# Performance work log

Measured on AMD Instinct MI355X. Metric: run time of the kernel, lower is better.

## Reference

```python
import jax, jax.numpy as jnp
import numpy as np

N_NODES = 100000
N_EDGES = 3200000
NFEAT = 512
HIDDEN = 256
NCLASS = 64
K = 10
ALPHA = 0.1


def setup_inputs() -> dict:
    key = jax.random.key(0)
    ks = jax.random.split(key, 5)
    x = jax.random.normal(ks[0], (N_NODES, NFEAT), dtype=jnp.float32)
    edge_index = jax.random.randint(ks[1], (2, N_EDGES), 0, N_NODES, dtype=jnp.int64)
    W1 = jax.random.normal(ks[2], (NFEAT, HIDDEN), dtype=jnp.float32) * (1.0 / np.sqrt(NFEAT))
    b1 = jnp.zeros((HIDDEN,), dtype=jnp.float32)
    W2 = jax.random.normal(ks[3], (HIDDEN, NCLASS), dtype=jnp.float32) * (1.0 / np.sqrt(HIDDEN))
    b2 = jnp.zeros((NCLASS,), dtype=jnp.float32)
    # PPR initialization of GPR coefficients: alpha*(1-alpha)^k, last = (1-alpha)^K
    temp_np = ALPHA * (1.0 - ALPHA) ** np.arange(K + 1)
    temp_np[-1] = (1.0 - ALPHA) ** K
    temp = jnp.asarray(temp_np, dtype=jnp.float32)
    return {"x": x, "edge_index": edge_index, "W1": W1, "b1": b1, "W2": W2, "b2": b2, "temp": temp}


def reference(x, edge_index, W1, b1, W2, b2, temp):
    N = x.shape[0]
    # --- gcn_norm: add self-loops, symmetric normalization ---
    loop = jnp.arange(N, dtype=edge_index.dtype)
    row = jnp.concatenate([edge_index[0], loop])  # source nodes
    col = jnp.concatenate([edge_index[1], loop])  # target nodes
    ones = jnp.ones(row.shape[0], dtype=x.dtype)
    deg = jax.ops.segment_sum(ones, col, num_segments=N)
    dinv = jnp.where(deg > 0, jax.lax.rsqrt(deg), jnp.zeros((), x.dtype))
    norm = dinv[row] * dinv[col]  # [E+N]

    # --- MLP (eval mode: dropout is identity) ---
    h = jax.nn.relu(x @ W1 + b1) @ W2 + b2  # [N, nclass]

    # --- GPR propagation: hidden = sum_k temp[k] * (Ahat^k h) ---
    hidden = h * temp[0]
    for k in range(K):
        h = jax.ops.segment_sum(norm[:, None] * h[row], col, num_segments=N)
        hidden = hidden + temp[k + 1] * h

    return jax.nn.log_softmax(hidden, axis=1)
```

## Files before the change

kernel.cpp:

```cpp
#include <hip/hip_runtime.h>
#include <hip/hip_bf16.h>
#include <math.h>

#define N_NODES 100000
#define N_EDGES 3200000
#define NFEAT   512
#define HIDDEN  256
#define NCLASS  64
#define K_HOPS  10
#define NPART   8
#define PART_SZ ((N_NODES + NPART - 1) / NPART)

typedef unsigned short bfbits;
typedef __attribute__((ext_vector_type(8))) short short8x;
typedef __attribute__((ext_vector_type(4))) float float4x;

__device__ __forceinline__ float bf2f(bfbits u) {
    union { unsigned int i; float f; } v; v.i = ((unsigned int)u) << 16; return v.f;
}
__device__ __forceinline__ bfbits f2bf(float f) {
    union { float f; unsigned int i; } v; v.f = f;
    unsigned int b = v.i + 0x7FFFu + ((v.i >> 16) & 1u);
    return (bfbits)(b >> 16);
}
__device__ __forceinline__ float2 unpack2(unsigned int u) {
    float2 r;
    union { unsigned int i; float f; } a, b;
    a.i = (u & 0xFFFFu) << 16; b.i = u & 0xFFFF0000u;
    r.x = a.f; r.y = b.f; return r;
}
__device__ __forceinline__ unsigned int pack2(float x, float y) {
    return ((unsigned int)f2bf(x)) | (((unsigned int)f2bf(y)) << 16);
}


__global__ void init_kernel(int* __restrict__ degi, int* __restrict__ cursor, int n) {
    int i = blockIdx.x * blockDim.x + threadIdx.x;
    if (i < n) { degi[i] = 1; cursor[i] = 0; }
}

__global__ void count_kernel(const int* __restrict__ col, int* __restrict__ degi, int e) {
    int i = blockIdx.x * blockDim.x + threadIdx.x;
    if (i < e) atomicAdd(&degi[col[i]], 1);
}

__global__ void dinv_kernel(const int* __restrict__ degi, float* __restrict__ dinv, int n) {
    int i = blockIdx.x * blockDim.x + threadIdx.x;
    if (i < n) dinv[i] = rsqrtf((float)degi[i]);
}

#define SCAN_NB 256
#define SCAN_NT 256

__global__ __launch_bounds__(SCAN_NT) void scan_phase1(const int* __restrict__ degi,
                                                       int* __restrict__ blocksums, int n) {
    int chunk = (n + SCAN_NB - 1) / SCAN_NB;
    int beg = blockIdx.x * chunk;
    int end = min(beg + chunk, n);
    int tid = threadIdx.x;
    int s = 0;
    for (int i = beg + tid; i < end; i += SCAN_NT) s += degi[i] - 1;
    __shared__ int wsum[SCAN_NT / 64];
#pragma unroll
    for (int o = 32; o > 0; o >>= 1) s += __shfl_xor(s, o, 64);
    if ((tid & 63) == 0) wsum[tid >> 6] = s;
    __syncthreads();
    if (tid == 0) {
        int t = 0;
#pragma unroll
        for (int w = 0; w < SCAN_NT / 64; ++w) t += wsum[w];
        blocksums[blockIdx.x] = t;
    }
}

__global__ __launch_bounds__(SCAN_NB) void scan_phase2(const int* __restrict__ blocksums,
                                                       int* __restrict__ blockbase) {
    __shared__ int t[SCAN_NB];
    int tid = threadIdx.x;
    t[tid] = blocksums[tid];
    __syncthreads();
    for (int d = 1; d < SCAN_NB; d <<= 1) {
        int v = (tid >= d) ? t[tid - d] : 0;
        __syncthreads();
        t[tid] += v;
        __syncthreads();
    }
    blockbase[tid] = (tid > 0) ? t[tid - 1] : 0;
}

__global__ __launch_bounds__(SCAN_NT) void scan_phase3(const int* __restrict__ degi,
                                                       const int* __restrict__ blockbase,
                                                       int* __restrict__ offs, int n) {
    __shared__ int tsum[SCAN_NT];
    int chunk = (n + SCAN_NB - 1) / SCAN_NB;
    int beg = blockIdx.x * chunk;
    int end = min(beg + chunk, n);
    int tid = threadIdx.x;
    int sub = (chunk + SCAN_NT - 1) / SCAN_NT;
    int tb = beg + tid * sub;
    int te = min(tb + sub, end);
    int s = 0;
    for (int i = tb; i < te; ++i) s += degi[i] - 1;
    tsum[tid] = s;
    __syncthreads();
    for (int d = 1; d < SCAN_NT; d <<= 1) {
        int v = (tid >= d) ? tsum[tid - d] : 0;
        __syncthreads();
        tsum[tid] += v;
        __syncthreads();
    }
    int run = blockbase[blockIdx.x] + ((tid > 0) ? tsum[tid - 1] : 0);
    for (int i = tb; i < te; ++i) { offs[i] = run; run += degi[i] - 1; }
    if (blockIdx.x == SCAN_NB - 1 && tid == SCAN_NT - 1)
        offs[n] = blockbase[blockIdx.x] + tsum[SCAN_NT - 1];
}

__global__ __launch_bounds__(256) void scatter_part(const int* __restrict__ row,
                                                    const int* __restrict__ col,
                                                    const int* __restrict__ offs,
                                                    int* __restrict__ cursor,
                                                    int* __restrict__ srcs, int e) {
    int part = blockIdx.x & (NPART - 1);
    int blk  = blockIdx.x >> 3;
    int nthr = (gridDim.x >> 3) * blockDim.x;
    int lo = part * PART_SZ, hi = lo + PART_SZ;
    for (int i = blk * blockDim.x + threadIdx.x; i < e; i += nthr) {
        int c = col[i];
        int r = row[i];
        if (c >= lo && c < hi) {
            int p = offs[c] + atomicAdd(&cursor[c], 1);
            srcs[p] = r;
        }
    }
}

__global__ __launch_bounds__(256) void transpose_cast(const float* __restrict__ src,
                                                      bfbits* __restrict__ dst,
                                                      int K, int N) {
    __shared__ float tile[32][33];
    int kt = blockIdx.x * 32, nt = blockIdx.y * 32;
    int c = threadIdx.x & 31, r0 = threadIdx.x >> 5;
#pragma unroll
    for (int i = 0; i < 4; ++i) {
        int r = r0 + i * 8;
        tile[r][c] = src[(size_t)(kt + r) * N + nt + c];
    }
    __syncthreads();
#pragma unroll
    for (int i = 0; i < 4; ++i) {
        int r = r0 + i * 8;
        dst[(size_t)(nt + r) * K + kt + c] = f2bf(tile[c][r]);
    }
}

#define LDP 40

__global__ __launch_bounds__(512) void gemm1_mfma(const float* __restrict__ X,
                                                  const bfbits* __restrict__ W1T,
                                                  const float* __restrict__ bias,
                                                  bfbits* __restrict__ H, int M) {
    __shared__ short x_lds[128 * LDP];
    __shared__ short w_lds[256 * LDP];
    int tid = threadIdx.x;
    int wave = tid >> 6, lane = tid & 63;
    int l15 = lane & 15, quad = lane >> 4;
    int fslot = wave & 3, nslot = wave >> 2;
    int m0 = blockIdx.x * 128;

    float4x acc[4][4];
#pragma unroll
    for (int i = 0; i < 4; ++i)
#pragma unroll
        for (int j = 0; j < 4; ++j) acc[i][j] = (float4x){0.f, 0.f, 0.f, 0.f};

    for (int kb = 0; kb < NFEAT; kb += 32) {
#pragma unroll
        for (int c = 0; c < 2; ++c) {
            int qid = tid + c * 512;
            int node = qid >> 3;
            int k0 = (qid & 7) * 4;
            int row = m0 + node;
            float4 v = make_float4(0.f, 0.f, 0.f, 0.f);
            if (row < M) v = *reinterpret_cast<const float4*>(X + (size_t)row * NFEAT + kb + k0);
            ushort4 u;
            u.x = f2bf(v.x); u.y = f2bf(v.y); u.z = f2bf(v.z); u.w = f2bf(v.w);
            *reinterpret_cast<ushort4*>(&x_lds[node * LDP + k0]) = u;
        }
#pragma unroll
        for (int c = 0; c < 2; ++c) {
            int qid = tid + c * 512;
            int feat = qid >> 2;
            int k0 = (qid & 3) * 8;
            uint4 w = *reinterpret_cast<const uint4*>(W1T + (size_t)feat * NFEAT + kb + k0);
            *reinterpret_cast<uint4*>(&w_lds[feat * LDP + k0]) = w;
        }
        __syncthreads();
        short8x af[4], bf[4];
#pragma unroll
        for (int t = 0; t < 4; ++t) {
            af[t] = *reinterpret_cast<const short8x*>(&w_lds[(fslot * 64 + t * 16 + l15) * LDP + quad * 8]);
            bf[t] = *reinterpret_cast<const short8x*>(&x_lds[(nslot * 64 + t * 16 + l15) * LDP + quad * 8]);
        }
#pragma unroll
        for (int ft = 0; ft < 4; ++ft)
#pragma unroll
            for (int nt = 0; nt < 4; ++nt)
                acc[ft][nt] = __builtin_amdgcn_mfma_f32_16x16x32_bf16(af[ft], bf[nt], acc[ft][nt], 0, 0, 0);
        __syncthreads();
    }
#pragma unroll
    for (int ft = 0; ft < 4; ++ft) {
        int f = fslot * 64 + ft * 16 + quad * 4;
        float4 b = *reinterpret_cast<const float4*>(bias + f);
#pragma unroll
        for (int nt = 0; nt < 4; ++nt) {
            int node = m0 + nslot * 64 + nt * 16 + l15;
            if (node >= M) continue;
            float4x a = acc[ft][nt];
            ushort4 u;
            u.x = f2bf(fmaxf(a.x + b.x, 0.f));
            u.y = f2bf(fmaxf(a.y + b.y, 0.f));
            u.z = f2bf(fmaxf(a.z + b.z, 0.f));
            u.w = f2bf(fmaxf(a.w + b.w, 0.f));
            *reinterpret_cast<ushort4*>(H + (size_t)node * HIDDEN + f) = u;
        }
    }
}

__global__ __launch_bounds__(256) void gemm2_mfma(const bfbits* __restrict__ Hm,
                                                  const bfbits* __restrict__ W2T,
                                                  const float* __restrict__ bias,
                                                  const float* __restrict__ dinv,
                                                  bfbits* __restrict__ g0,
                                                  float* __restrict__ S,
                                                  const float* __restrict__ temp, int M) {
    __shared__ short h_lds[256 * LDP];
    __shared__ short w_lds[64 * LDP];
    int tid = threadIdx.x;
    int wave = tid >> 6, lane = tid & 63;
    int l15 = lane & 15, quad = lane >> 4;
    int nslot = wave;
    int m0 = blockIdx.x * 256;

    float4x acc[4][4];
#pragma unroll
    for (int i = 0; i < 4; ++i)
#pragma unroll
        for (int j = 0; j < 4; ++j) acc[i][j] = (float4x){0.f, 0.f, 0.f, 0.f};

    for (int kb = 0; kb < HIDDEN; kb += 32) {
#pragma unroll
        for (int c = 0; c < 4; ++c) {
            int qid = tid + c * 256;
            int node = qid >> 2;
            int k0 = (qid & 3) * 8;
            int row = m0 + node;
            uint4 v = make_uint4(0u, 0u, 0u, 0u);
            if (row < M) v = *reinterpret_cast<const uint4*>(Hm + (size_t)row * HIDDEN + kb + k0);
            *reinterpret_cast<uint4*>(&h_lds[node * LDP + k0]) = v;
        }
        {
            int feat = tid >> 2;
            int k0 = (tid & 3) * 8;
            uint4 w = *reinterpret_cast<const uint4*>(W2T + (size_t)feat * HIDDEN + kb + k0);
            *reinterpret_cast<uint4*>(&w_lds[feat * LDP + k0]) = w;
        }
        __syncthreads();
        short8x af[4], bf[4];
#pragma unroll
        for (int t = 0; t < 4; ++t) {
            af[t] = *reinterpret_cast<const short8x*>(&w_lds[(t * 16 + l15) * LDP + quad * 8]);
            bf[t] = *reinterpret_cast<const short8x*>(&h_lds[(nslot * 64 + t * 16 + l15) * LDP + quad * 8]);
        }
#pragma unroll
        for (int ft = 0; ft < 4; ++ft)
#pragma unroll
            for (int nt = 0; nt < 4; ++nt)
                acc[ft][nt] = __builtin_amdgcn_mfma_f32_16x16x32_bf16(af[ft], bf[nt], acc[ft][nt], 0, 0, 0);
        __syncthreads();
    }
    float t0 = temp[0];
#pragma unroll
    for (int nt = 0; nt < 4; ++nt) {
        int node = m0 + nslot * 64 + nt * 16 + l15;
        if (node >= M) continue;
        float di = dinv[node];
        float s0 = t0 / di;
#pragma unroll
        for (int ft = 0; ft < 4; ++ft) {
            int f = ft * 16 + quad * 4;
            float4 b = *reinterpret_cast<const float4*>(bias + f);
            float4x a = acc[ft][nt];
            float4 v = make_float4(a.x + b.x, a.y + b.y, a.z + b.z, a.w + b.w);
            ushort4 u;
            u.x = f2bf(di * v.x); u.y = f2bf(di * v.y);
            u.z = f2bf(di * v.z); u.w = f2bf(di * v.w);
            *reinterpret_cast<ushort4*>(g0 + (size_t)node * NCLASS + f) = u;
            float4 sv = make_float4(s0 * v.x, s0 * v.y, s0 * v.z, s0 * v.w);
            *reinterpret_cast<float4*>(S + (size_t)node * 64 + f) = sv;
        }
    }
}

__global__ __launch_bounds__(256) void propagate_kernel(const int* __restrict__ offs,
                                                        const int* __restrict__ srcs,
                                                        const float* __restrict__ dinv,
                                                        const uint2* __restrict__ gin,
                                                        uint2* __restrict__ gout,
                                                        float* __restrict__ S,
                                                        const float* __restrict__ temp,
                                                        int kidx, int n) {
    int node = (blockIdx.x * blockDim.x + threadIdx.x) >> 6;
    int lane = threadIdx.x & 63;
    if (node >= n) return;
    int q = lane >> 4, sub = lane & 15;
    float tk = temp[kidx];
    int beg = offs[node], end = offs[node + 1];

    uint2 gs = gin[(size_t)node * 16 + sub];
    float4 acc = make_float4(0.f, 0.f, 0.f, 0.f);
    if (q == 0) {
        float2 lo = unpack2(gs.x), hi = unpack2(gs.y);
        acc = make_float4(lo.x, lo.y, hi.x, hi.y);
    }

    int e = beg;
    for (; e + 16 <= end; e += 16) {
#pragma unroll
        for (int j = 0; j < 4; ++j) {
            int s = srcs[e + j * 4 + q];
            uint2 u = gin[(size_t)s * 16 + sub];
            float2 lo = unpack2(u.x), hi = unpack2(u.y);
            acc.x += lo.x; acc.y += lo.y; acc.z += hi.x; acc.w += hi.y;
        }
    }
    for (; e < end; e += 4) {
        int idx = e + q;
        int sidx = (idx < end) ? idx : e;
        int s = srcs[sidx];
        uint2 u = gin[(size_t)s * 16 + sub];
        if (idx < end) {
            float2 lo = unpack2(u.x), hi = unpack2(u.y);
            acc.x += lo.x; acc.y += lo.y; acc.z += hi.x; acc.w += hi.y;
        }
    }

    acc.x += __shfl_xor(acc.x, 16, 64); acc.y += __shfl_xor(acc.y, 16, 64);
    acc.z += __shfl_xor(acc.z, 16, 64); acc.w += __shfl_xor(acc.w, 16, 64);
    acc.x += __shfl_xor(acc.x, 32, 64); acc.y += __shfl_xor(acc.y, 32, 64);
    acc.z += __shfl_xor(acc.z, 32, 64); acc.w += __shfl_xor(acc.w, 32, 64);

    if (q == 0) {
        float di = dinv[node];
        float dd = di * di;
        gout[(size_t)node * 16 + sub] =
            make_uint2(pack2(dd * acc.x, dd * acc.y), pack2(dd * acc.z, dd * acc.w));
        float4* Sp = reinterpret_cast<float4*>(S + (size_t)node * 64 + sub * 4);
        float4 sv = *Sp;
        sv.x += tk * acc.x; sv.y += tk * acc.y;
        sv.z += tk * acc.z; sv.w += tk * acc.w;
        *Sp = sv;
    }
}

__global__ __launch_bounds__(256) void logsoftmax_kernel(const float* __restrict__ S,
                                                         const float* __restrict__ dinv,
                                                         float* __restrict__ out, int n) {
    int node = (blockIdx.x * blockDim.x + threadIdx.x) >> 6;
    int lane = threadIdx.x & 63;
    if (node >= n) return;
    float v = dinv[node] * S[(size_t)node * 64 + lane];
    float m = v;
#pragma unroll
    for (int o = 32; o > 0; o >>= 1) m = fmaxf(m, __shfl_xor(m, o, 64));
    float ex = expf(v - m);
    float s = ex;
#pragma unroll
    for (int o = 32; o > 0; o >>= 1) s += __shfl_xor(s, o, 64);
    out[(size_t)node * 64 + lane] = v - m - logf(s);
}


extern "C" void kernel_launch(void* const* d_in, const int* in_sizes, int n_in,
                              void* d_out, int out_size, void* d_ws, size_t ws_size,
                              hipStream_t stream) {
    const float* x    = (const float*)d_in[0];
    const int*   ei   = (const int*)d_in[1];
    const int*   row  = ei;
    const int*   col  = ei + N_EDGES;
    const float* W1   = (const float*)d_in[2];
    const float* b1   = (const float*)d_in[3];
    const float* W2   = (const float*)d_in[4];
    const float* b2   = (const float*)d_in[5];
    const float* temp = (const float*)d_in[6];
    float*       out  = (float*)d_out;

    char* ws = (char*)d_ws;
    size_t off = 0;
    auto alloc = [&](size_t bytes) -> void* {
        void* p = ws + off;
        off += (bytes + 255) & ~(size_t)255;
        return p;
    };
    int*    degi   = (int*)   alloc((size_t)N_NODES * 4);
    float*  dinv   = (float*) alloc((size_t)N_NODES * 4);
    int*    offs   = (int*)   alloc((size_t)(N_NODES + 1) * 4);
    int*    cursor = (int*)   alloc((size_t)N_NODES * 4);
    int*    srcs   = (int*)   alloc((size_t)N_EDGES * 4);
    int*    bsums  = (int*)   alloc((size_t)SCAN_NB * 4);
    int*    bbase  = (int*)   alloc((size_t)SCAN_NB * 4);
    bfbits* W1T    = (bfbits*)alloc((size_t)HIDDEN * NFEAT * 2);
    bfbits* W2T    = (bfbits*)alloc((size_t)NCLASS * HIDDEN * 2);
    bfbits* h_mlp  = (bfbits*)alloc((size_t)N_NODES * HIDDEN * 2);
    bfbits* g_a    = (bfbits*)alloc((size_t)N_NODES * NCLASS * 2);
    bfbits* g_b    = (bfbits*)alloc((size_t)N_NODES * NCLASS * 2);
    float*  S      = (float*) alloc((size_t)N_NODES * NCLASS * 4);

    init_kernel<<<(N_NODES + 255) / 256, 256, 0, stream>>>(degi, cursor, N_NODES);
    count_kernel<<<(N_EDGES + 255) / 256, 256, 0, stream>>>(col, degi, N_EDGES);
    dinv_kernel<<<(N_NODES + 255) / 256, 256, 0, stream>>>(degi, dinv, N_NODES);
    scan_phase1<<<SCAN_NB, SCAN_NT, 0, stream>>>(degi, bsums, N_NODES);
    scan_phase2<<<1, SCAN_NB, 0, stream>>>(bsums, bbase);
    scan_phase3<<<SCAN_NB, SCAN_NT, 0, stream>>>(degi, bbase, offs, N_NODES);
    scatter_part<<<2048, 256, 0, stream>>>(row, col, offs, cursor, srcs, N_EDGES);

    dim3 gt1(NFEAT / 32, HIDDEN / 32);
    transpose_cast<<<gt1, 256, 0, stream>>>(W1, W1T, NFEAT, HIDDEN);
    dim3 gt2(HIDDEN / 32, NCLASS / 32);
    transpose_cast<<<gt2, 256, 0, stream>>>(W2, W2T, HIDDEN, NCLASS);

    gemm1_mfma<<<(N_NODES + 127) / 128, 512, 0, stream>>>(x, W1T, b1, h_mlp, N_NODES);
    gemm2_mfma<<<(N_NODES + 255) / 256, 256, 0, stream>>>(h_mlp, W2T, b2, dinv, g_a, S,
                                                          temp, N_NODES);

    int pgrid = (N_NODES * 64 + 255) / 256;
    for (int k = 0; k < K_HOPS; ++k) {
        bfbits* gi = (k & 1) ? g_b : g_a;
        bfbits* go = (k & 1) ? g_a : g_b;
        propagate_kernel<<<pgrid, 256, 0, stream>>>(offs, srcs, dinv,
                                                    (const uint2*)gi, (uint2*)go, S,
                                                    temp, k + 1, N_NODES);
    }

    logsoftmax_kernel<<<pgrid, 256, 0, stream>>>(S, dinv, out, N_NODES);
}
```

Before: 1.357 ms.

## Bucket CSR neighbor lists by source-node range to improve gather locality

Builds the CSR with four virtual buckets per destination node, keyed by which quarter of the source-node range each edge comes from. Within a node's neighbor list, sources are then grouped by region, so concurrent gathers in the propagation hops hit a smaller working set in cache. Edge index loads in the count and scatter kernels become nontemporal. In exchange the count, scan and cursor arrays grow fourfold and the count kernel also has to read the row indices.

```diff
diff --git a/kernel.cpp b/kernel.cpp
--- a/kernel.cpp
+++ b/kernel.cpp
@@ -10,6 +10,9 @@
 #define K_HOPS  10
 #define NPART   8
 #define PART_SZ ((N_NODES + NPART - 1) / NPART)
+#define NTILE   4
+#define TQ      25000
+#define NVIRT   (N_NODES * NTILE)
 
 typedef unsigned short bfbits;
 typedef __attribute__((ext_vector_type(8))) short short8x;
@@ -34,32 +37,41 @@
 }
 
 
-__global__ void init_kernel(int* __restrict__ degi, int* __restrict__ cursor, int n) {
+__global__ void init_kernel(int* __restrict__ bcnt, int* __restrict__ cursor, int n) {
     int i = blockIdx.x * blockDim.x + threadIdx.x;
-    if (i < n) { degi[i] = 1; cursor[i] = 0; }
-}
-
-__global__ void count_kernel(const int* __restrict__ col, int* __restrict__ degi, int e) {
+    if (i < n) { bcnt[i] = 0; cursor[i] = 0; }
+}
+
+__global__ void count_kernel(const int* __restrict__ row, const int* __restrict__ col,
+                             int* __restrict__ bcnt, int e) {
     int i = blockIdx.x * blockDim.x + threadIdx.x;
-    if (i < e) atomicAdd(&degi[col[i]], 1);
-}
-
-__global__ void dinv_kernel(const int* __restrict__ degi, float* __restrict__ dinv, int n) {
+    if (i < e) {
+        int r = __builtin_nontemporal_load(row + i);
+        int c = __builtin_nontemporal_load(col + i);
+        atomicAdd(&bcnt[c * NTILE + r / TQ], 1);
+    }
+}
+
+__global__ void dinv_kernel(const int* __restrict__ bcnt, float* __restrict__ dinv, int n) {
     int i = blockIdx.x * blockDim.x + threadIdx.x;
-    if (i < n) dinv[i] = rsqrtf((float)degi[i]);
+    if (i < n) {
+        int d = 1 + bcnt[i * NTILE] + bcnt[i * NTILE + 1] + bcnt[i * NTILE + 2]
+                  + bcnt[i * NTILE + 3];
+        dinv[i] = rsqrtf((float)d);
+    }
 }
 
 #define SCAN_NB 256
 #define SCAN_NT 256
 
-__global__ __launch_bounds__(SCAN_NT) void scan_phase1(const int* __restrict__ degi,
+__global__ __launch_bounds__(SCAN_NT) void scan_phase1(const int* __restrict__ bcnt,
                                                        int* __restrict__ blocksums, int n) {
     int chunk = (n + SCAN_NB - 1) / SCAN_NB;
     int beg = blockIdx.x * chunk;
     int end = min(beg + chunk, n);
     int tid = threadIdx.x;
     int s = 0;
-    for (int i = beg + tid; i < end; i += SCAN_NT) s += degi[i] - 1;
+    for (int i = beg + tid; i < end; i += SCAN_NT) s += bcnt[i];
     __shared__ int wsum[SCAN_NT / 64];
 #pragma unroll
     for (int o = 32; o > 0; o >>= 1) s += __shfl_xor(s, o, 64);
@@ -88,7 +100,7 @@
     blockbase[tid] = (tid > 0) ? t[tid - 1] : 0;
 }
 
-__global__ __launch_bounds__(SCAN_NT) void scan_phase3(const int* __restrict__ degi,
+__global__ __launch_bounds__(SCAN_NT) void scan_phase3(const int* __restrict__ bcnt,
                                                        const int* __restrict__ blockbase,
                                                        int* __restrict__ offs, int n) {
     __shared__ int tsum[SCAN_NT];
@@ -100,7 +112,7 @@
     int tb = beg + tid * sub;
     int te = min(tb + sub, end);
     int s = 0;
-    for (int i = tb; i < te; ++i) s += degi[i] - 1;
+    for (int i = tb; i < te; ++i) s += bcnt[i];
     tsum[tid] = s;
     __syncthreads();
     for (int d = 1; d < SCAN_NT; d <<= 1) {
@@ -110,14 +122,14 @@
         __syncthreads();
     }
     int run = blockbase[blockIdx.x] + ((tid > 0) ? tsum[tid - 1] : 0);
-    for (int i = tb; i < te; ++i) { offs[i] = run; run += degi[i] - 1; }
+    for (int i = tb; i < te; ++i) { offs[i] = run; run += bcnt[i]; }
     if (blockIdx.x == SCAN_NB - 1 && tid == SCAN_NT - 1)
         offs[n] = blockbase[blockIdx.x] + tsum[SCAN_NT - 1];
 }
 
 __global__ __launch_bounds__(256) void scatter_part(const int* __restrict__ row,
                                                     const int* __restrict__ col,
-                                                    const int* __restrict__ offs,
+                                                    const int* __restrict__ offs2,
                                                     int* __restrict__ cursor,
                                                     int* __restrict__ srcs, int e) {
     int part = blockIdx.x & (NPART - 1);
@@ -125,10 +137,11 @@
     int nthr = (gridDim.x >> 3) * blockDim.x;
     int lo = part * PART_SZ, hi = lo + PART_SZ;
     for (int i = blk * blockDim.x + threadIdx.x; i < e; i += nthr) {
-        int c = col[i];
-        int r = row[i];
+        int c = __builtin_nontemporal_load(col + i);
+        int r = __builtin_nontemporal_load(row + i);
         if (c >= lo && c < hi) {
-            int p = offs[c] + atomicAdd(&cursor[c], 1);
+            int vk = c * NTILE + r / TQ;
+            int p = offs2[vk] + atomicAdd(&cursor[vk], 1);
             srcs[p] = r;
         }
     }
@@ -302,7 +315,7 @@
     }
 }
 
-__global__ __launch_bounds__(256) void propagate_kernel(const int* __restrict__ offs,
+__global__ __launch_bounds__(256) void propagate_kernel(const int* __restrict__ offs2,
                                                         const int* __restrict__ srcs,
                                                         const float* __restrict__ dinv,
                                                         const uint2* __restrict__ gin,
@@ -315,7 +328,7 @@
     if (node >= n) return;
     int q = lane >> 4, sub = lane & 15;
     float tk = temp[kidx];
-    int beg = offs[node], end = offs[node + 1];
+    int beg = offs2[node * NTILE], end = offs2[node * NTILE + NTILE];
 
     uint2 gs = gin[(size_t)node * 16 + sub];
     float4 acc = make_float4(0.f, 0.f, 0.f, 0.f);
@@ -402,10 +415,10 @@
         off += (bytes + 255) & ~(size_t)255;
         return p;
     };
-    int*    degi   = (int*)   alloc((size_t)N_NODES * 4);
+    int*    bcnt   = (int*)   alloc((size_t)NVIRT * 4);
+    int*    offs2  = (int*)   alloc((size_t)(NVIRT + 1) * 4);
+    int*    cursor = (int*)   alloc((size_t)NVIRT * 4);
     float*  dinv   = (float*) alloc((size_t)N_NODES * 4);
-    int*    offs   = (int*)   alloc((size_t)(N_NODES + 1) * 4);
-    int*    cursor = (int*)   alloc((size_t)N_NODES * 4);
     int*    srcs   = (int*)   alloc((size_t)N_EDGES * 4);
     int*    bsums  = (int*)   alloc((size_t)SCAN_NB * 4);
     int*    bbase  = (int*)   alloc((size_t)SCAN_NB * 4);
@@ -416,13 +429,13 @@
     bfbits* g_b    = (bfbits*)alloc((size_t)N_NODES * NCLASS * 2);
     float*  S      = (float*) alloc((size_t)N_NODES * NCLASS * 4);
 
-    init_kernel<<<(N_NODES + 255) / 256, 256, 0, stream>>>(degi, cursor, N_NODES);
-    count_kernel<<<(N_EDGES + 255) / 256, 256, 0, stream>>>(col, degi, N_EDGES);
-    dinv_kernel<<<(N_NODES + 255) / 256, 256, 0, stream>>>(degi, dinv, N_NODES);
-    scan_phase1<<<SCAN_NB, SCAN_NT, 0, stream>>>(degi, bsums, N_NODES);
+    init_kernel<<<(NVIRT + 255) / 256, 256, 0, stream>>>(bcnt, cursor, NVIRT);
+    count_kernel<<<(N_EDGES + 255) / 256, 256, 0, stream>>>(row, col, bcnt, N_EDGES);
+    dinv_kernel<<<(N_NODES + 255) / 256, 256, 0, stream>>>(bcnt, dinv, N_NODES);
+    scan_phase1<<<SCAN_NB, SCAN_NT, 0, stream>>>(bcnt, bsums, NVIRT);
     scan_phase2<<<1, SCAN_NB, 0, stream>>>(bsums, bbase);
-    scan_phase3<<<SCAN_NB, SCAN_NT, 0, stream>>>(degi, bbase, offs, N_NODES);
-    scatter_part<<<2048, 256, 0, stream>>>(row, col, offs, cursor, srcs, N_EDGES);
+    scan_phase3<<<SCAN_NB, SCAN_NT, 0, stream>>>(bcnt, bbase, offs2, NVIRT);
+    scatter_part<<<2048, 256, 0, stream>>>(row, col, offs2, cursor, srcs, N_EDGES);
 
     dim3 gt1(NFEAT / 32, HIDDEN / 32);
     transpose_cast<<<gt1, 256, 0, stream>>>(W1, W1T, NFEAT, HIDDEN);
@@ -437,7 +450,7 @@
     for (int k = 0; k < K_HOPS; ++k) {
         bfbits* gi = (k & 1) ? g_b : g_a;
         bfbits* go = (k & 1) ? g_a : g_b;
-        propagate_kernel<<<pgrid, 256, 0, stream>>>(offs, srcs, dinv,
+        propagate_kernel<<<pgrid, 256, 0, stream>>>(offs2, srcs, dinv,
                                                     (const uint2*)gi, (uint2*)go, S,
                                                     temp, k + 1, N_NODES);
     }
```

Result: no change. 1.375 ms (+1.4%).
